# Kernel optimization log

Hardware: AMD Instinct MI355X
Metric: run time of the kernel (lower is better)

## Reference

```python
import jax, jax.numpy as jnp
import numpy as np

DIM, D_INNER, D_STATE, D_CONV, DT_RANK = 768, 1536, 16, 4, 48
B, L = 2, 1024

def setup_inputs() -> dict:
    key = jax.random.key(0)
    ks = jax.random.split(key, 10)
    s = lambda fan: 1.0 / np.sqrt(fan)
    return {
        'x': jax.random.normal(ks[0], (B, L, DIM), jnp.float32),
        'ln_w': jnp.ones((DIM,), jnp.float32),
        'ln_b': jnp.zeros((DIM,), jnp.float32),
        'in_proj_w': jax.random.normal(ks[1], (2 * D_INNER, DIM), jnp.float32) * s(DIM),
        'conv_w': jax.random.normal(ks[2], (D_INNER, D_CONV), jnp.float32) * s(D_CONV),
        'conv_b': jnp.zeros((D_INNER,), jnp.float32),
        'x_proj_w': jax.random.normal(ks[3], (DT_RANK + 2 * D_STATE, D_INNER), jnp.float32) * s(D_INNER),
        'dt_proj_w': jax.random.normal(ks[4], (D_INNER, DT_RANK), jnp.float32) * s(DT_RANK),
        'dt_proj_b': jax.random.normal(ks[5], (D_INNER,), jnp.float32) * 0.1 - 4.0,  # softplus ~ small dt
        'A_log': jnp.log(jnp.broadcast_to(jnp.arange(1, D_STATE + 1, dtype=jnp.float32), (D_INNER, D_STATE))),
        'D_param': jnp.ones((D_INNER,), jnp.float32),
        'out_proj_w': jax.random.normal(ks[6], (DIM, D_INNER), jnp.float32) * s(D_INNER),
    }

def _silu(v):
    return v * jax.nn.sigmoid(v)

def reference(x, ln_w, ln_b, in_proj_w, conv_w, conv_b, x_proj_w,
              dt_proj_w, dt_proj_b, A_log, D_param, out_proj_w):
    Bb, Ll, _ = x.shape
    # LayerNorm (eps=1e-5, torch default)
    mu = jnp.mean(x, -1, keepdims=True)
    var = jnp.mean(jnp.square(x - mu), -1, keepdims=True)
    xn = (x - mu) * jax.lax.rsqrt(var + 1e-5) * ln_w + ln_b
    # in_proj -> (B,L,2*d_inner), split into x-branch and gate z
    xz = xn @ in_proj_w.T
    xm, z = jnp.split(xz, 2, axis=-1)
    # causal depthwise conv1d, kernel D_CONV, left-pad D_CONV-1
    xp = jnp.pad(xm, ((0, 0), (D_CONV - 1, 0), (0, 0)))
    xc = conv_b + sum(xp[:, k:k + Ll, :] * conv_w[:, k] for k in range(D_CONV))
    u = _silu(xc)  # (B,L,d_inner)
    # input-dependent dt, B, C
    dbc = u @ x_proj_w.T
    dt, Bm, Cm = jnp.split(dbc, [DT_RANK, DT_RANK + D_STATE], axis=-1)
    delta = jax.nn.softplus(dt @ dt_proj_w.T + dt_proj_b)  # (B,L,d_inner)
    A = -jnp.exp(A_log)  # (d_inner, d_state), negative
    dA = jnp.exp(delta[..., None] * A)                      # (B,L,D,N)
    dBu = (delta * u)[..., None] * Bm[:, :, None, :]        # (B,L,D,N)
    # linear recurrence h_t = dA_t * h_{t-1} + dBu_t via associative scan
    def comb(e1, e2):
        a1, b1 = e1
        a2, b2 = e2
        return a1 * a2, a2 * b1 + b2
    _, h = jax.lax.associative_scan(comb, (dA, dBu), axis=1)
    y = jnp.einsum('bldn,bln->bld', h, Cm) + u * D_param
    y = y * _silu(z)
    return y @ out_proj_w.T
```

## Files before the change

kernel.cpp:

```cpp
#include <hip/hip_runtime.h>
#include <hip/hip_bf16.h>

#define BATCH 2
#define SEQ   1024
#define DIM   768
#define DI    1536
#define DS    16
#define DCONV 4
#define DTR   48
#define XZW   (2*DI)
#define DBCW  (DTR+2*DS)
#define MROWS (BATCH*SEQ)
#define NCHUNK 32
#define CLEN  (SEQ/NCHUNK)
#define XP_KS 8
#define OP_KS 4
#define XPN   128

typedef unsigned short ushort_t;
typedef __attribute__((ext_vector_type(8))) short short8;
typedef __attribute__((ext_vector_type(4))) float f32x4;

__device__ __forceinline__ float sigmoidf_(float x) {
    return 1.f / (1.f + __expf(-x));
}

__device__ __forceinline__ ushort_t f2bf(float x) {
    union { float f; unsigned u; } c{x};
    unsigned r = c.u + 0x7FFF + ((c.u >> 16) & 1);
    return (ushort_t)(r >> 16);
}

__device__ __forceinline__ float bf2f(ushort_t v) {
    union { unsigned u; float f; } c{(unsigned)v << 16};
    return c.f;
}

__device__ __forceinline__ void gload16(const void* g, void* lds) {
    __builtin_amdgcn_global_load_lds(
        (const __attribute__((address_space(1))) void*)g,
        (__attribute__((address_space(3))) void*)lds,
        16, 0, 0);
}

#define PREP_W1 ((XZW*DIM)/8)
#define PREP_W2 ((DIM*DI)/8)
#define PREP_A  (DS*DI)
#define PREP_X  (XPN*DI)
#define PREP_DT (DI*64)
__global__ __launch_bounds__(256) void prep_all(const float* __restrict__ in_proj_w,
                                                const float* __restrict__ out_proj_w,
                                                const float* __restrict__ A_log,
                                                const float* __restrict__ x_proj_w,
                                                const float* __restrict__ dt_proj_w,
                                                ushort_t* __restrict__ w_in_bf,
                                                ushort_t* __restrict__ w_out_bf,
                                                float* __restrict__ aT,
                                                ushort_t* __restrict__ xpw_pad,
                                                ushort_t* __restrict__ dtw_bf)
{
    int i = blockIdx.x * 256 + threadIdx.x;
    if (i < PREP_W1) {
        int j = i * 8;
        float4 a = *(const float4*)(in_proj_w + j);
        float4 b = *(const float4*)(in_proj_w + j + 4);
        ushort_t o[8] = { f2bf(a.x), f2bf(a.y), f2bf(a.z), f2bf(a.w),
                          f2bf(b.x), f2bf(b.y), f2bf(b.z), f2bf(b.w) };
        *(ushort4*)(w_in_bf + j)     = *(ushort4*)o;
        *(ushort4*)(w_in_bf + j + 4) = *(ushort4*)(o + 4);
        return;
    }
    i -= PREP_W1;
    if (i < PREP_W2) {
        int j = i * 8;
        float4 a = *(const float4*)(out_proj_w + j);
        float4 b = *(const float4*)(out_proj_w + j + 4);
        ushort_t o[8] = { f2bf(a.x), f2bf(a.y), f2bf(a.z), f2bf(a.w),
                          f2bf(b.x), f2bf(b.y), f2bf(b.z), f2bf(b.w) };
        *(ushort4*)(w_out_bf + j)     = *(ushort4*)o;
        *(ushort4*)(w_out_bf + j + 4) = *(ushort4*)(o + 4);
        return;
    }
    i -= PREP_W2;
    if (i < PREP_A) {
        int n = i / DI, d = i % DI;
        aT[i] = -__expf(A_log[d * DS + n]) * 1.44269504f;
        return;
    }
    i -= PREP_A;
    if (i < PREP_X) {
        int r = i / DI, c = i % DI;
        xpw_pad[i] = (r < DBCW) ? f2bf(x_proj_w[r * DI + c]) : (ushort_t)0;
        return;
    }
    i -= PREP_X;
    if (i < PREP_DT) {
        int r = i / 64, c = i % 64;
        dtw_bf[i] = (c < DTR) ? f2bf(dt_proj_w[r * DTR + c]) : (ushort_t)0;
    }
}

__global__ __launch_bounds__(256) void reduce_sk4(const float4* __restrict__ part,
                                                  float4* __restrict__ out,
                                                  int count4, int nslices)
{
    int i = blockIdx.x * 256 + threadIdx.x;
    if (i >= count4) return;
    float4 s = part[i];
    for (int z = 1; z < nslices; ++z) {
        float4 p = part[(size_t)z * count4 + i];
        s.x += p.x; s.y += p.y; s.z += p.z; s.w += p.w;
    }
    out[i] = s;
}

__global__ __launch_bounds__(256) void reduce_dbc(const float* __restrict__ part,
                                                  float* __restrict__ dbc,
                                                  ushort_t* __restrict__ dtb)
{
    int i = blockIdx.x * 256 + threadIdx.x;
    if (i >= MROWS * XPN) return;
    float s = 0.f;
    #pragma unroll
    for (int z = 0; z < XP_KS; ++z)
        s += part[(size_t)z * MROWS * XPN + i];
    int r = i / XPN, c = i % XPN;
    if (c < DBCW) dbc[(size_t)r * DBCW + c] = s;
    if (c < 64)   dtb[(size_t)r * 64 + c] = (c < DTR) ? f2bf(s) : (ushort_t)0;
}

__global__ __launch_bounds__(256) void ln_kernel(const float* __restrict__ x,
                                                 const float* __restrict__ w,
                                                 const float* __restrict__ b,
                                                 ushort_t* __restrict__ xn)
{
    __shared__ float part[8];
    int row = blockIdx.x;
    const float* xr = x + (size_t)row * DIM;
    ushort_t* o = xn + (size_t)row * DIM;
    int tid = threadIdx.x;
    int lane = tid & 63, wid = tid >> 6;

    float v0 = xr[tid], v1 = xr[tid + 256], v2 = xr[tid + 512];
    float s = v0 + v1 + v2;
    #pragma unroll
    for (int off = 32; off > 0; off >>= 1) s += __shfl_xor(s, off);
    if (lane == 0) part[wid] = s;
    __syncthreads();
    float mu = (part[0] + part[1] + part[2] + part[3]) * (1.f / DIM);

    float d0 = v0 - mu, d1 = v1 - mu, d2 = v2 - mu;
    float q = d0 * d0 + d1 * d1 + d2 * d2;
    #pragma unroll
    for (int off = 32; off > 0; off >>= 1) q += __shfl_xor(q, off);
    if (lane == 0) part[4 + wid] = q;
    __syncthreads();
    float rstd = rsqrtf((part[4] + part[5] + part[6] + part[7]) * (1.f / DIM) + 1e-5f);

    o[tid]       = f2bf(d0 * rstd * w[tid]       + b[tid]);
    o[tid + 256] = f2bf(d1 * rstd * w[tid + 256] + b[tid + 256]);
    o[tid + 512] = f2bf(d2 * rstd * w[tid + 512] + b[tid + 512]);
}

__global__ __launch_bounds__(256) void gemm_bf16_obf(const ushort_t* __restrict__ A,
                                                     const ushort_t* __restrict__ W,
                                                     ushort_t* __restrict__ C,
                                                     int N, int K)
{
    __shared__ __align__(16) ushort_t As[128 * 32];
    __shared__ __align__(16) ushort_t Bs[128 * 32];

    int tid = threadIdx.x;
    int wave = tid >> 6, lane = tid & 63;
    int wr = wave >> 1, wc = wave & 1;
    int l15 = lane & 15, kb = lane >> 4;
    int m0 = blockIdx.y * 128, n0 = blockIdx.x * 128;

    f32x4 acc[4][4] = {};

    for (int k0 = 0; k0 < K; k0 += 32) {
        #pragma unroll
        for (int i = 0; i < 2; ++i) {
            int cbase = i * 256 + wave * 64;
            int c = cbase + lane;
            int row = c >> 2;
            int col = (c & 3) * 8;
            gload16(A + (size_t)(m0 + row) * K + k0 + col, (char*)As + (size_t)cbase * 16);
            gload16(W + (size_t)(n0 + row) * K + k0 + col, (char*)Bs + (size_t)cbase * 16);
        }
        __syncthreads();

        short8 af[4], bfr[4];
        #pragma unroll
        for (int m = 0; m < 4; ++m)
            af[m] = *(const short8*)&As[(wr * 64 + m * 16 + l15) * 32 + kb * 8];
        #pragma unroll
        for (int n = 0; n < 4; ++n)
            bfr[n] = *(const short8*)&Bs[(wc * 64 + n * 16 + l15) * 32 + kb * 8];

        #pragma unroll
        for (int m = 0; m < 4; ++m)
            #pragma unroll
            for (int n = 0; n < 4; ++n)
                acc[m][n] = __builtin_amdgcn_mfma_f32_16x16x32_bf16(af[m], bfr[n], acc[m][n], 0, 0, 0);

        __syncthreads();
    }

    int r0 = m0 + wr * 64 + kb * 4;
    int c0 = n0 + wc * 64 + l15;
    #pragma unroll
    for (int m = 0; m < 4; ++m)
        #pragma unroll
        for (int n = 0; n < 4; ++n) {
            int rr = r0 + m * 16;
            int cc = c0 + n * 16;
            #pragma unroll
            for (int r = 0; r < 4; ++r)
                C[(size_t)(rr + r) * N + cc] = f2bf(acc[m][n][r]);
        }
}

__global__ __launch_bounds__(256) void gemm_bf16_sk(const ushort_t* __restrict__ A,
                                                    const ushort_t* __restrict__ W,
                                                    float* __restrict__ Cpart,
                                                    int N, int Ktot, int Kslice, int M)
{
    __shared__ __align__(16) ushort_t As[128 * 32];
    __shared__ __align__(16) ushort_t Bs[128 * 32];

    int tid = threadIdx.x;
    int wave = tid >> 6, lane = tid & 63;
    int wr = wave >> 1, wc = wave & 1;
    int l15 = lane & 15, kb = lane >> 4;
    int m0 = blockIdx.y * 128, n0 = blockIdx.x * 128;
    int kbase = blockIdx.z * Kslice;
    float* C = Cpart + (size_t)blockIdx.z * M * N;

    f32x4 acc[4][4] = {};

    for (int k0 = kbase; k0 < kbase + Kslice; k0 += 32) {
        #pragma unroll
        for (int i = 0; i < 2; ++i) {
            int cbase = i * 256 + wave * 64;
            int c = cbase + lane;
            int row = c >> 2;
            int col = (c & 3) * 8;
            gload16(A + (size_t)(m0 + row) * Ktot + k0 + col, (char*)As + (size_t)cbase * 16);
            gload16(W + (size_t)(n0 + row) * Ktot + k0 + col, (char*)Bs + (size_t)cbase * 16);
        }
        __syncthreads();

        short8 af[4], bfr[4];
        #pragma unroll
        for (int m = 0; m < 4; ++m)
            af[m] = *(const short8*)&As[(wr * 64 + m * 16 + l15) * 32 + kb * 8];
        #pragma unroll
        for (int n = 0; n < 4; ++n)
            bfr[n] = *(const short8*)&Bs[(wc * 64 + n * 16 + l15) * 32 + kb * 8];

        #pragma unroll
        for (int m = 0; m < 4; ++m)
            #pragma unroll
            for (int n = 0; n < 4; ++n)
                acc[m][n] = __builtin_amdgcn_mfma_f32_16x16x32_bf16(af[m], bfr[n], acc[m][n], 0, 0, 0);

        __syncthreads();
    }

    int r0 = m0 + wr * 64 + kb * 4;
    int c0 = n0 + wc * 64 + l15;
    #pragma unroll
    for (int m = 0; m < 4; ++m)
        #pragma unroll
        for (int n = 0; n < 4; ++n) {
            int rr = r0 + m * 16;
            int cc = c0 + n * 16;
            #pragma unroll
            for (int r = 0; r < 4; ++r)
                C[(size_t)(rr + r) * N + cc] = acc[m][n][r];
        }
}

__global__ __launch_bounds__(256) void gemm_dt(const ushort_t* __restrict__ A,
                                               const ushort_t* __restrict__ W,
                                               const float* __restrict__ bias,
                                               float* __restrict__ C)
{
    __shared__ __align__(16) ushort_t As[128 * 32];
    __shared__ __align__(16) ushort_t Bs[128 * 32];

    int tid = threadIdx.x;
    int wave = tid >> 6, lane = tid & 63;
    int wr = wave >> 1, wc = wave & 1;
    int l15 = lane & 15, kb = lane >> 4;
    int m0 = blockIdx.y * 128, n0 = blockIdx.x * 128;

    f32x4 acc[4][4] = {};

    #pragma unroll
    for (int k0 = 0; k0 < 64; k0 += 32) {
        #pragma unroll
        for (int i = 0; i < 2; ++i) {
            int cbase = i * 256 + wave * 64;
            int c = cbase + lane;
            int row = c >> 2;
            int col = (c & 3) * 8;
            gload16(A + (size_t)(m0 + row) * 64 + k0 + col, (char*)As + (size_t)cbase * 16);
            gload16(W + (size_t)(n0 + row) * 64 + k0 + col, (char*)Bs + (size_t)cbase * 16);
        }
        __syncthreads();

        short8 af[4], bfr[4];
        #pragma unroll
        for (int m = 0; m < 4; ++m)
            af[m] = *(const short8*)&As[(wr * 64 + m * 16 + l15) * 32 + kb * 8];
        #pragma unroll
        for (int n = 0; n < 4; ++n)
            bfr[n] = *(const short8*)&Bs[(wc * 64 + n * 16 + l15) * 32 + kb * 8];

        #pragma unroll
        for (int m = 0; m < 4; ++m)
            #pragma unroll
            for (int n = 0; n < 4; ++n)
                acc[m][n] = __builtin_amdgcn_mfma_f32_16x16x32_bf16(af[m], bfr[n], acc[m][n], 0, 0, 0);

        __syncthreads();
    }

    int r0 = m0 + wr * 64 + kb * 4;
    int c0 = n0 + wc * 64 + l15;
    #pragma unroll
    for (int m = 0; m < 4; ++m)
        #pragma unroll
        for (int n = 0; n < 4; ++n) {
            int rr = r0 + m * 16;
            int cc = c0 + n * 16;
            float bv = bias[cc];
            #pragma unroll
            for (int r = 0; r < 4; ++r) {
                float v = acc[m][n][r] + bv;
                v = (v > 20.f) ? v : log1pf(__expf(v));
                C[(size_t)(rr + r) * DI + cc] = v;
            }
        }
}

__global__ __launch_bounds__(256) void conv_silu_kernel(const ushort_t* __restrict__ xzb,
                                                        const float* __restrict__ cw,
                                                        const float* __restrict__ cb,
                                                        ushort_t* __restrict__ u_bf)
{
    int idx = blockIdx.x * 256 + threadIdx.x;
    int d4 = idx % (DI / 4);
    int bt = idx / (DI / 4);
    int t = bt % SEQ;
    int b = bt / SEQ;
    int d = d4 * 4;

    float4 w0 = *(const float4*)(cw + (d + 0) * 4);
    float4 w1 = *(const float4*)(cw + (d + 1) * 4);
    float4 w2 = *(const float4*)(cw + (d + 2) * 4);
    float4 w3 = *(const float4*)(cw + (d + 3) * 4);
    const float* wp[4] = { (const float*)&w0, (const float*)&w1,
                           (const float*)&w2, (const float*)&w3 };

    float4 acc = *(const float4*)(cb + d);
    #pragma unroll
    for (int k = 0; k < DCONV; ++k) {
        int tt = t - (DCONV - 1) + k;
        if (tt >= 0) {
            ushort4 xv = *(const ushort4*)(xzb + (size_t)(b * SEQ + tt) * XZW + d);
            acc.x += bf2f(xv.x) * wp[0][k];
            acc.y += bf2f(xv.y) * wp[1][k];
            acc.z += bf2f(xv.z) * wp[2][k];
            acc.w += bf2f(xv.w) * wp[3][k];
        }
    }
    acc.x *= sigmoidf_(acc.x);
    acc.y *= sigmoidf_(acc.y);
    acc.z *= sigmoidf_(acc.z);
    acc.w *= sigmoidf_(acc.w);
    ushort4 ob = { f2bf(acc.x), f2bf(acc.y), f2bf(acc.z), f2bf(acc.w) };
    *(ushort4*)(u_bf + (size_t)(b * SEQ + t) * DI + d) = ob;
}

__global__ __launch_bounds__(256) void scan_p1(const float* __restrict__ delta,
                                               const ushort_t* __restrict__ u,
                                               const float* __restrict__ dbc,
                                               const float* __restrict__ aT,
                                               float* __restrict__ Pw,
                                               float* __restrict__ Sw)
{
    __shared__ float Bs[4][CLEN][DS];
    int tid = threadIdx.x;
    int lane = tid & 63, w = tid >> 6;
    int d = blockIdx.x * 64 + lane;
    int chunk = blockIdx.y * 4 + w;
    int b = blockIdx.z;
    int t0 = chunk * CLEN;

    #pragma unroll
    for (int i = 0; i < 2; ++i) {
        int idx = i * 64 + lane;
        int tl = idx >> 2, c = idx & 3;
        *(float4*)&Bs[w][tl][c * 4] =
            *(const float4*)(dbc + (size_t)(b * SEQ + t0 + tl) * DBCW + DTR + c * 4);
    }

    float a[DS];
    #pragma unroll
    for (int n = 0; n < DS; ++n) a[n] = aT[n * DI + d];

    __syncthreads();

    float P[DS], S[DS];
    #pragma unroll
    for (int n = 0; n < DS; ++n) { P[n] = 1.f; S[n] = 0.f; }

    const float* dp    = delta + ((size_t)b * SEQ + t0) * DI + d;
    const ushort_t* up = u     + ((size_t)b * SEQ + t0) * DI + d;
    #pragma unroll 4
    for (int j = 0; j < CLEN; ++j) {
        float dlt = dp[(size_t)j * DI];
        float uu  = bf2f(up[(size_t)j * DI]);
        float dltu = dlt * uu;
        #pragma unroll
        for (int n = 0; n < DS; ++n) {
            float dA = exp2f(dlt * a[n]);
            P[n] *= dA;
            S[n] = dA * S[n] + dltu * Bs[w][j][n];
        }
    }

    size_t base = (((size_t)b * NCHUNK + chunk) * DS) * DI + d;
    #pragma unroll
    for (int n = 0; n < DS; ++n) {
        Pw[base + (size_t)n * DI] = P[n];
        Sw[base + (size_t)n * DI] = S[n];
    }
}

__global__ __launch_bounds__(256) void scan_comb(const float* __restrict__ Pw,
                                                 const float* __restrict__ Sw,
                                                 float* __restrict__ Hin)
{
    int d = blockIdx.x * 256 + threadIdx.x;
    int n = blockIdx.y, b = blockIdx.z;
    float h = 0.f;
    for (int c = 0; c < NCHUNK; ++c) {
        size_t idx = (((size_t)b * NCHUNK + c) * DS + n) * DI + d;
        Hin[idx] = h;
        h = Pw[idx] * h + Sw[idx];
    }
}

__global__ __launch_bounds__(256) void scan_p3(const float* __restrict__ delta,
                                               const ushort_t* __restrict__ u,
                                               const float* __restrict__ dbc,
                                               const ushort_t* __restrict__ xzb,
                                               const float* __restrict__ aT,
                                               const float* __restrict__ Dp,
                                               const float* __restrict__ Hin,
                                               ushort_t* __restrict__ y)
{
    __shared__ float Bs[4][CLEN][2 * DS];
    int tid = threadIdx.x;
    int lane = tid & 63, w = tid >> 6;
    int d = blockIdx.x * 64 + lane;
    int chunk = blockIdx.y * 4 + w;
    int b = blockIdx.z;
    int t0 = chunk * CLEN;

    #pragma unroll
    for (int i = 0; i < 4; ++i) {
        int idx = i * 64 + lane;
        int tl = idx >> 3, c = idx & 7;
        *(float4*)&Bs[w][tl][c * 4] =
            *(const float4*)(dbc + (size_t)(b * SEQ + t0 + tl) * DBCW + DTR + c * 4);
    }

    float a[DS], h[DS];
    #pragma unroll
    for (int n = 0; n < DS; ++n) a[n] = aT[n * DI + d];
    size_t hbase = (((size_t)b * NCHUNK + chunk) * DS) * DI + d;
    #pragma unroll
    for (int n = 0; n < DS; ++n) h[n] = Hin[hbase + (size_t)n * DI];

    float Dd = Dp[d];
    __syncthreads();

    const float* dp    = delta + ((size_t)b * SEQ + t0) * DI + d;
    const ushort_t* up = u     + ((size_t)b * SEQ + t0) * DI + d;
    const ushort_t* zp = xzb   + ((size_t)b * SEQ + t0) * XZW + DI + d;
    ushort_t* yp       = y     + ((size_t)b * SEQ + t0) * DI + d;

    #pragma unroll 2
    for (int j = 0; j < CLEN; ++j) {
        float dlt = dp[(size_t)j * DI];
        float uu  = bf2f(up[(size_t)j * DI]);
        float dltu = dlt * uu;
        #pragma unroll
        for (int n = 0; n < DS; ++n) {
            float dA = exp2f(dlt * a[n]);
            h[n] = dA * h[n] + dltu * Bs[w][j][n];
        }
        float p0 = 0.f, p1 = 0.f, p2 = 0.f, p3 = 0.f;
        #pragma unroll
        for (int n = 0; n < DS; n += 4) {
            p0 += h[n]     * Bs[w][j][DS + n];
            p1 += h[n + 1] * Bs[w][j][DS + n + 1];
            p2 += h[n + 2] * Bs[w][j][DS + n + 2];
            p3 += h[n + 3] * Bs[w][j][DS + n + 3];
        }
        float p = (p0 + p1) + (p2 + p3);
        float z = bf2f(zp[(size_t)j * XZW]);
        float yv = (p + uu * Dd) * (z * sigmoidf_(z));
        yp[(size_t)j * DI] = f2bf(yv);
    }
}

extern "C" void kernel_launch(void* const* d_in, const int* in_sizes, int n_in,
                              void* d_out, int out_size, void* d_ws, size_t ws_size,
                              hipStream_t stream) {
    const float* x         = (const float*)d_in[0];
    const float* ln_w      = (const float*)d_in[1];
    const float* ln_b      = (const float*)d_in[2];
    const float* in_proj_w = (const float*)d_in[3];
    const float* conv_w    = (const float*)d_in[4];
    const float* conv_b    = (const float*)d_in[5];
    const float* x_proj_w  = (const float*)d_in[6];
    const float* dt_proj_w = (const float*)d_in[7];
    const float* dt_proj_b = (const float*)d_in[8];
    const float* A_log     = (const float*)d_in[9];
    const float* D_param   = (const float*)d_in[10];
    const float* out_proj_w= (const float*)d_in[11];
    float* out = (float*)d_out;

    char* ws = (char*)d_ws;
    size_t off = 0;
    auto alloc = [&](size_t bytes) { void* p = ws + off; off += (bytes + 255) & ~255ull; return p; };

    ushort_t* xn_bf   = (ushort_t*)alloc((size_t)MROWS * DIM * 2);
    ushort_t* w_in_bf = (ushort_t*)alloc((size_t)XZW * DIM * 2);
    ushort_t* w_out_bf= (ushort_t*)alloc((size_t)DIM * DI * 2);
    ushort_t* y_bf    = (ushort_t*)alloc((size_t)MROWS * DI * 2);
    ushort_t* u_bf    = (ushort_t*)alloc((size_t)MROWS * DI * 2);
    ushort_t* xpw_pad = (ushort_t*)alloc((size_t)XPN * DI * 2);
    ushort_t* dtw_bf  = (ushort_t*)alloc((size_t)DI * 64 * 2);
    ushort_t* dtb     = (ushort_t*)alloc((size_t)MROWS * 64 * 2);
    ushort_t* xzb     = (ushort_t*)alloc((size_t)MROWS * XZW * 2);
    float* dbc   = (float*)alloc((size_t)MROWS * DBCW * 4);
    float* delta = (float*)alloc((size_t)MROWS * DI * 4);
    float* aT    = (float*)alloc((size_t)DS * DI * 4);
    float* xpart = (float*)alloc((size_t)XP_KS * MROWS * XPN * 4);
    float* opart = (float*)alloc((size_t)OP_KS * MROWS * DIM * 4);

    size_t cvol = (size_t)BATCH * NCHUNK * DS * DI;
    float* Pw  = opart;
    float* Sw  = opart + cvol;
    float* Hin = opart + 2 * cvol;

    hipLaunchKernelGGL(prep_all,
                       dim3((PREP_W1 + PREP_W2 + PREP_A + PREP_X + PREP_DT + 255) / 256),
                       dim3(256), 0, stream,
                       in_proj_w, out_proj_w, A_log, x_proj_w, dt_proj_w,
                       w_in_bf, w_out_bf, aT, xpw_pad, dtw_bf);

    hipLaunchKernelGGL(ln_kernel, dim3(MROWS), dim3(256), 0, stream, x, ln_w, ln_b, xn_bf);

    hipLaunchKernelGGL(gemm_bf16_obf, dim3(XZW / 128, MROWS / 128), dim3(256), 0, stream,
                       xn_bf, w_in_bf, xzb, XZW, DIM);

    hipLaunchKernelGGL(conv_silu_kernel, dim3((MROWS * DI / 4) / 256), dim3(256), 0, stream,
                       xzb, conv_w, conv_b, u_bf);

    hipLaunchKernelGGL(gemm_bf16_sk, dim3(XPN / 128, MROWS / 128, XP_KS), dim3(256), 0, stream,
                       u_bf, xpw_pad, xpart, XPN, DI, DI / XP_KS, MROWS);
    hipLaunchKernelGGL(reduce_dbc, dim3((MROWS * XPN + 255) / 256), dim3(256), 0, stream,
                       xpart, dbc, dtb);

    hipLaunchKernelGGL(gemm_dt, dim3(DI / 128, MROWS / 128), dim3(256), 0, stream,
                       dtb, dtw_bf, dt_proj_b, delta);

    hipLaunchKernelGGL(scan_p1, dim3(DI / 64, NCHUNK / 4, BATCH), dim3(256), 0, stream,
                       delta, u_bf, dbc, aT, Pw, Sw);
    hipLaunchKernelGGL(scan_comb, dim3(DI / 256, DS, BATCH), dim3(256), 0, stream,
                       Pw, Sw, Hin);
    hipLaunchKernelGGL(scan_p3, dim3(DI / 64, NCHUNK / 4, BATCH), dim3(256), 0, stream,
                       delta, u_bf, dbc, xzb, aT, D_param, Hin, y_bf);

    hipLaunchKernelGGL(gemm_bf16_sk, dim3(DIM / 128, MROWS / 128, OP_KS), dim3(256), 0, stream,
                       y_bf, w_out_bf, opart, DIM, DI, DI / OP_KS, MROWS);
    hipLaunchKernelGGL(reduce_sk4, dim3((MROWS * DIM / 4 + 255) / 256), dim3(256), 0, stream,
                       (const float4*)opart, (float4*)out, MROWS * DIM / 4, OP_KS);
}
```

Before: 178.9 us.

## Fuse LayerNorm into prep kernel, bf16 delta, swizzled K64 in_proj GEMM, trim dbc writes

Merges the weight-conversion prep kernel and LayerNorm into a single launch. The in_proj GEMM now uses K=64 tiles with an XOR-swizzled LDS layout to cut bank conflicts and halve the barrier count. The softplus delta is stored as bf16 rather than fp32, halving its traffic in both scan passes at some precision cost. The x_proj split-K GEMM skips padded output columns, and its reduction skips columns beyond DBCW, to save memory traffic.

```diff
diff --git a/kernel.cpp b/kernel.cpp
--- a/kernel.cpp
+++ b/kernel.cpp
@@ -48,17 +48,51 @@
 #define PREP_A  (DS*DI)
 #define PREP_X  (XPN*DI)
 #define PREP_DT (DI*64)
-__global__ __launch_bounds__(256) void prep_all(const float* __restrict__ in_proj_w,
-                                                const float* __restrict__ out_proj_w,
-                                                const float* __restrict__ A_log,
-                                                const float* __restrict__ x_proj_w,
-                                                const float* __restrict__ dt_proj_w,
-                                                ushort_t* __restrict__ w_in_bf,
-                                                ushort_t* __restrict__ w_out_bf,
-                                                float* __restrict__ aT,
-                                                ushort_t* __restrict__ xpw_pad,
-                                                ushort_t* __restrict__ dtw_bf)
-{
+#define PREP_BLOCKS ((PREP_W1+PREP_W2+PREP_A+PREP_X+PREP_DT+255)/256)
+__global__ __launch_bounds__(256) void prep_ln(const float* __restrict__ in_proj_w,
+                                               const float* __restrict__ out_proj_w,
+                                               const float* __restrict__ A_log,
+                                               const float* __restrict__ x_proj_w,
+                                               const float* __restrict__ dt_proj_w,
+                                               const float* __restrict__ x,
+                                               const float* __restrict__ ln_w,
+                                               const float* __restrict__ ln_b,
+                                               ushort_t* __restrict__ w_in_bf,
+                                               ushort_t* __restrict__ w_out_bf,
+                                               float* __restrict__ aT,
+                                               ushort_t* __restrict__ xpw_pad,
+                                               ushort_t* __restrict__ dtw_bf,
+                                               ushort_t* __restrict__ xn)
+{
+    __shared__ float part[8];
+    if (blockIdx.x >= PREP_BLOCKS) {
+        int row = blockIdx.x - PREP_BLOCKS;
+        const float* xr = x + (size_t)row * DIM;
+        ushort_t* o = xn + (size_t)row * DIM;
+        int tid = threadIdx.x;
+        int lane = tid & 63, wid = tid >> 6;
+
+        float v0 = xr[tid], v1 = xr[tid + 256], v2 = xr[tid + 512];
+        float s = v0 + v1 + v2;
+        #pragma unroll
+        for (int off = 32; off > 0; off >>= 1) s += __shfl_xor(s, off);
+        if (lane == 0) part[wid] = s;
+        __syncthreads();
+        float mu = (part[0] + part[1] + part[2] + part[3]) * (1.f / DIM);
+
+        float d0 = v0 - mu, d1 = v1 - mu, d2 = v2 - mu;
+        float q = d0 * d0 + d1 * d1 + d2 * d2;
+        #pragma unroll
+        for (int off = 32; off > 0; off >>= 1) q += __shfl_xor(q, off);
+        if (lane == 0) part[4 + wid] = q;
+        __syncthreads();
+        float rstd = rsqrtf((part[4] + part[5] + part[6] + part[7]) * (1.f / DIM) + 1e-5f);
+
+        o[tid]       = f2bf(d0 * rstd * ln_w[tid]       + ln_b[tid]);
+        o[tid + 256] = f2bf(d1 * rstd * ln_w[tid + 256] + ln_b[tid + 256]);
+        o[tid + 512] = f2bf(d2 * rstd * ln_w[tid + 512] + ln_b[tid + 512]);
+        return;
+    }
     int i = blockIdx.x * 256 + threadIdx.x;
     if (i < PREP_W1) {
         int j = i * 8;
@@ -120,46 +154,14 @@
 {
     int i = blockIdx.x * 256 + threadIdx.x;
     if (i >= MROWS * XPN) return;
+    int r = i / XPN, c = i % XPN;
+    if (c >= DBCW) return;
     float s = 0.f;
     #pragma unroll
     for (int z = 0; z < XP_KS; ++z)
         s += part[(size_t)z * MROWS * XPN + i];
-    int r = i / XPN, c = i % XPN;
-    if (c < DBCW) dbc[(size_t)r * DBCW + c] = s;
-    if (c < 64)   dtb[(size_t)r * 64 + c] = (c < DTR) ? f2bf(s) : (ushort_t)0;
-}
-
-__global__ __launch_bounds__(256) void ln_kernel(const float* __restrict__ x,
-                                                 const float* __restrict__ w,
-                                                 const float* __restrict__ b,
-                                                 ushort_t* __restrict__ xn)
-{
-    __shared__ float part[8];
-    int row = blockIdx.x;
-    const float* xr = x + (size_t)row * DIM;
-    ushort_t* o = xn + (size_t)row * DIM;
-    int tid = threadIdx.x;
-    int lane = tid & 63, wid = tid >> 6;
-
-    float v0 = xr[tid], v1 = xr[tid + 256], v2 = xr[tid + 512];
-    float s = v0 + v1 + v2;
-    #pragma unroll
-    for (int off = 32; off > 0; off >>= 1) s += __shfl_xor(s, off);
-    if (lane == 0) part[wid] = s;
-    __syncthreads();
-    float mu = (part[0] + part[1] + part[2] + part[3]) * (1.f / DIM);
-
-    float d0 = v0 - mu, d1 = v1 - mu, d2 = v2 - mu;
-    float q = d0 * d0 + d1 * d1 + d2 * d2;
-    #pragma unroll
-    for (int off = 32; off > 0; off >>= 1) q += __shfl_xor(q, off);
-    if (lane == 0) part[4 + wid] = q;
-    __syncthreads();
-    float rstd = rsqrtf((part[4] + part[5] + part[6] + part[7]) * (1.f / DIM) + 1e-5f);
-
-    o[tid]       = f2bf(d0 * rstd * w[tid]       + b[tid]);
-    o[tid + 256] = f2bf(d1 * rstd * w[tid + 256] + b[tid + 256]);
-    o[tid + 512] = f2bf(d2 * rstd * w[tid + 512] + b[tid + 512]);
+    dbc[(size_t)r * DBCW + c] = s;
+    if (c < 64) dtb[(size_t)r * 64 + c] = (c < DTR) ? f2bf(s) : (ushort_t)0;
 }
 
 __global__ __launch_bounds__(256) void gemm_bf16_obf(const ushort_t* __restrict__ A,
@@ -167,8 +169,8 @@
                                                      ushort_t* __restrict__ C,
                                                      int N, int K)
 {
-    __shared__ __align__(16) ushort_t As[128 * 32];
-    __shared__ __align__(16) ushort_t Bs[128 * 32];
+    __shared__ __align__(16) ushort_t As[128 * 64];
+    __shared__ __align__(16) ushort_t Bs[128 * 64];
 
     int tid = threadIdx.x;
     int wave = tid >> 6, lane = tid & 63;
@@ -178,32 +180,37 @@
 
     f32x4 acc[4][4] = {};
 
-    for (int k0 = 0; k0 < K; k0 += 32) {
-        #pragma unroll
-        for (int i = 0; i < 2; ++i) {
+    for (int k0 = 0; k0 < K; k0 += 64) {
+        #pragma unroll
+        for (int i = 0; i < 4; ++i) {
             int cbase = i * 256 + wave * 64;
             int c = cbase + lane;
-            int row = c >> 2;
-            int col = (c & 3) * 8;
-            gload16(A + (size_t)(m0 + row) * K + k0 + col, (char*)As + (size_t)cbase * 16);
-            gload16(W + (size_t)(n0 + row) * K + k0 + col, (char*)Bs + (size_t)cbase * 16);
-        }
-        __syncthreads();
-
-        short8 af[4], bfr[4];
-        #pragma unroll
-        for (int m = 0; m < 4; ++m)
-            af[m] = *(const short8*)&As[(wr * 64 + m * 16 + l15) * 32 + kb * 8];
-        #pragma unroll
-        for (int n = 0; n < 4; ++n)
-            bfr[n] = *(const short8*)&Bs[(wc * 64 + n * 16 + l15) * 32 + kb * 8];
-
-        #pragma unroll
-        for (int m = 0; m < 4; ++m)
+            int row = c >> 3;
+            int sg = (c & 7) ^ (row & 7);
+            gload16(A + (size_t)(m0 + row) * K + k0 + sg * 8, (char*)As + (size_t)cbase * 16);
+            gload16(W + (size_t)(n0 + row) * K + k0 + sg * 8, (char*)Bs + (size_t)cbase * 16);
+        }
+        __syncthreads();
+
+        #pragma unroll
+        for (int kk = 0; kk < 2; ++kk) {
+            short8 af[4], bfr[4];
             #pragma unroll
-            for (int n = 0; n < 4; ++n)
-                acc[m][n] = __builtin_amdgcn_mfma_f32_16x16x32_bf16(af[m], bfr[n], acc[m][n], 0, 0, 0);
-
+            for (int m = 0; m < 4; ++m) {
+                int row = wr * 64 + m * 16 + l15;
+                af[m] = *(const short8*)&As[row * 64 + (((kk * 4 + kb) ^ (row & 7)) * 8)];
+            }
+            #pragma unroll
+            for (int n = 0; n < 4; ++n) {
+                int row = wc * 64 + n * 16 + l15;
+                bfr[n] = *(const short8*)&Bs[row * 64 + (((kk * 4 + kb) ^ (row & 7)) * 8)];
+            }
+            #pragma unroll
+            for (int m = 0; m < 4; ++m)
+                #pragma unroll
+                for (int n = 0; n < 4; ++n)
+                    acc[m][n] = __builtin_amdgcn_mfma_f32_16x16x32_bf16(af[m], bfr[n], acc[m][n], 0, 0, 0);
+        }
         __syncthreads();
     }
 
@@ -224,7 +231,7 @@
 __global__ __launch_bounds__(256) void gemm_bf16_sk(const ushort_t* __restrict__ A,
                                                     const ushort_t* __restrict__ W,
                                                     float* __restrict__ Cpart,
-                                                    int N, int Ktot, int Kslice, int M)
+                                                    int N, int Ktot, int Kslice, int M, int Nw)
 {
     __shared__ __align__(16) ushort_t As[128 * 32];
     __shared__ __align__(16) ushort_t Bs[128 * 32];
@@ -276,16 +283,18 @@
         for (int n = 0; n < 4; ++n) {
             int rr = r0 + m * 16;
             int cc = c0 + n * 16;
-            #pragma unroll
-            for (int r = 0; r < 4; ++r)
-                C[(size_t)(rr + r) * N + cc] = acc[m][n][r];
+            if (cc < Nw) {
+                #pragma unroll
+                for (int r = 0; r < 4; ++r)
+                    C[(size_t)(rr + r) * N + cc] = acc[m][n][r];
+            }
         }
 }
 
 __global__ __launch_bounds__(256) void gemm_dt(const ushort_t* __restrict__ A,
                                                const ushort_t* __restrict__ W,
                                                const float* __restrict__ bias,
-                                               float* __restrict__ C)
+                                               ushort_t* __restrict__ C)
 {
     __shared__ __align__(16) ushort_t As[128 * 32];
     __shared__ __align__(16) ushort_t Bs[128 * 32];
@@ -341,7 +350,7 @@
             for (int r = 0; r < 4; ++r) {
                 float v = acc[m][n][r] + bv;
                 v = (v > 20.f) ? v : log1pf(__expf(v));
-                C[(size_t)(rr + r) * DI + cc] = v;
+                C[(size_t)(rr + r) * DI + cc] = f2bf(v);
             }
         }
 }
@@ -385,7 +394,7 @@
     *(ushort4*)(u_bf + (size_t)(b * SEQ + t) * DI + d) = ob;
 }
 
-__global__ __launch_bounds__(256) void scan_p1(const float* __restrict__ delta,
+__global__ __launch_bounds__(256) void scan_p1(const ushort_t* __restrict__ delta,
                                                const ushort_t* __restrict__ u,
                                                const float* __restrict__ dbc,
                                                const float* __restrict__ aT,
@@ -418,11 +427,11 @@
     #pragma unroll
     for (int n = 0; n < DS; ++n) { P[n] = 1.f; S[n] = 0.f; }
 
-    const float* dp    = delta + ((size_t)b * SEQ + t0) * DI + d;
+    const ushort_t* dp = delta + ((size_t)b * SEQ + t0) * DI + d;
     const ushort_t* up = u     + ((size_t)b * SEQ + t0) * DI + d;
     #pragma unroll 4
     for (int j = 0; j < CLEN; ++j) {
-        float dlt = dp[(size_t)j * DI];
+        float dlt = bf2f(dp[(size_t)j * DI]);
         float uu  = bf2f(up[(size_t)j * DI]);
         float dltu = dlt * uu;
         #pragma unroll
@@ -455,7 +464,7 @@
     }
 }
 
-__global__ __launch_bounds__(256) void scan_p3(const float* __restrict__ delta,
+__global__ __launch_bounds__(256) void scan_p3(const ushort_t* __restrict__ delta,
                                                const ushort_t* __restrict__ u,
                                                const float* __restrict__ dbc,
                                                const ushort_t* __restrict__ xzb,
@@ -490,14 +499,14 @@
     float Dd = Dp[d];
     __syncthreads();
 
-    const float* dp    = delta + ((size_t)b * SEQ + t0) * DI + d;
+    const ushort_t* dp = delta + ((size_t)b * SEQ + t0) * DI + d;
     const ushort_t* up = u     + ((size_t)b * SEQ + t0) * DI + d;
     const ushort_t* zp = xzb   + ((size_t)b * SEQ + t0) * XZW + DI + d;
     ushort_t* yp       = y     + ((size_t)b * SEQ + t0) * DI + d;
 
     #pragma unroll 2
     for (int j = 0; j < CLEN; ++j) {
-        float dlt = dp[(size_t)j * DI];
+        float dlt = bf2f(dp[(size_t)j * DI]);
         float uu  = bf2f(up[(size_t)j * DI]);
         float dltu = dlt * uu;
         #pragma unroll
@@ -550,8 +559,8 @@
     ushort_t* dtw_bf  = (ushort_t*)alloc((size_t)DI * 64 * 2);
     ushort_t* dtb     = (ushort_t*)alloc((size_t)MROWS * 64 * 2);
     ushort_t* xzb     = (ushort_t*)alloc((size_t)MROWS * XZW * 2);
+    ushort_t* delta_bf= (ushort_t*)alloc((size_t)MROWS * DI * 2);
     float* dbc   = (float*)alloc((size_t)MROWS * DBCW * 4);
-    float* delta = (float*)alloc((size_t)MROWS * DI * 4);
     float* aT    = (float*)alloc((size_t)DS * DI * 4);
     float* xpart = (float*)alloc((size_t)XP_KS * MROWS * XPN * 4);
     float* opart = (float*)alloc((size_t)OP_KS * MROWS * DIM * 4);
@@ -561,13 +570,10 @@
     float* Sw  = opart + cvol;
     float* Hin = opart + 2 * cvol;
 
-    hipLaunchKernelGGL(prep_all,
-                       dim3((PREP_W1 + PREP_W2 + PREP_A + PREP_X + PREP_DT + 255) / 256),
-                       dim3(256), 0, stream,
+    hipLaunchKernelGGL(prep_ln, dim3(PREP_BLOCKS + MROWS), dim3(256), 0, stream,
                        in_proj_w, out_proj_w, A_log, x_proj_w, dt_proj_w,
-                       w_in_bf, w_out_bf, aT, xpw_pad, dtw_bf);
-
-    hipLaunchKernelGGL(ln_kernel, dim3(MROWS), dim3(256), 0, stream, x, ln_w, ln_b, xn_bf);
+                       x, ln_w, ln_b,
+                       w_in_bf, w_out_bf, aT, xpw_pad, dtw_bf, xn_bf);
 
     hipLaunchKernelGGL(gemm_bf16_obf, dim3(XZW / 128, MROWS / 128), dim3(256), 0, stream,
                        xn_bf, w_in_bf, xzb, XZW, DIM);
@@ -576,22 +582,22 @@
                        xzb, conv_w, conv_b, u_bf);
 
     hipLaunchKernelGGL(gemm_bf16_sk, dim3(XPN / 128, MROWS / 128, XP_KS), dim3(256), 0, stream,
-                       u_bf, xpw_pad, xpart, XPN, DI, DI / XP_KS, MROWS);
+                       u_bf, xpw_pad, xpart, XPN, DI, DI / XP_KS, MROWS, DBCW);
     hipLaunchKernelGGL(reduce_dbc, dim3((MROWS * XPN + 255) / 256), dim3(256), 0, stream,
                        xpart, dbc, dtb);
 
     hipLaunchKernelGGL(gemm_dt, dim3(DI / 128, MROWS / 128), dim3(256), 0, stream,
-                       dtb, dtw_bf, dt_proj_b, delta);
+                       dtb, dtw_bf, dt_proj_b, delta_bf);
 
     hipLaunchKernelGGL(scan_p1, dim3(DI / 64, NCHUNK / 4, BATCH), dim3(256), 0, stream,
-                       delta, u_bf, dbc, aT, Pw, Sw);
+                       delta_bf, u_bf, dbc, aT, Pw, Sw);
     hipLaunchKernelGGL(scan_comb, dim3(DI / 256, DS, BATCH), dim3(256), 0, stream,
                        Pw, Sw, Hin);
     hipLaunchKernelGGL(scan_p3, dim3(DI / 64, NCHUNK / 4, BATCH), dim3(256), 0, stream,
-                       delta, u_bf, dbc, xzb, aT, D_param, Hin, y_bf);
+                       delta_bf, u_bf, dbc, xzb, aT, D_param, Hin, y_bf);
 
     hipLaunchKernelGGL(gemm_bf16_sk, dim3(DIM / 128, MROWS / 128, OP_KS), dim3(256), 0, stream,
-                       y_bf, w_out_bf, opart, DIM, DI, DI / OP_KS, MROWS);
+                       y_bf, w_out_bf, opart, DIM, DI, DI / OP_KS, MROWS, DIM);
     hipLaunchKernelGGL(reduce_sk4, dim3((MROWS * DIM / 4 + 255) / 256), dim3(256), 0, stream,
                        (const float4*)opart, (float4*)out, MROWS * DIM / 4, OP_KS);
 }
```

Result: faster. 170.7 us (-4.6%).
